# Kernel optimization log

Measured on AMD Instinct MI355X. Metric: run time of the kernel, lower is better.

## Reference

```python
import jax, jax.numpy as jnp
import numpy as np

E = 1024
H = 16
DH = E // H
FF = 4 * E
EPS = 1e-5


def _layer_norm(x, g, b):
    mu = jnp.mean(x, axis=-1, keepdims=True)
    var = jnp.var(x, axis=-1, keepdims=True)
    return (x - mu) * jax.lax.rsqrt(var + EPS) * g + b


def setup_inputs() -> dict:
    key = jax.random.key(0)
    ks = jax.random.split(key, 12)
    B, S = 2, 2048
    s_e = 1.0 / np.sqrt(E)
    s_f = 1.0 / np.sqrt(FF)
    return {
        "hidden_states": jax.random.normal(ks[0], (B, S, E), jnp.float32),
        "attention_mask": jnp.zeros((B, S), jnp.float32),
        "position_bias": jax.random.normal(ks[1], (H, S, S), jnp.float32) * 0.1,
        "Wq": jax.random.normal(ks[2], (E, E), jnp.float32) * s_e,
        "bq": jnp.zeros((E,), jnp.float32),
        "Wk": jax.random.normal(ks[3], (E, E), jnp.float32) * s_e,
        "bk": jnp.zeros((E,), jnp.float32),
        "Wv": jax.random.normal(ks[4], (E, E), jnp.float32) * s_e,
        "bv": jnp.zeros((E,), jnp.float32),
        "Wo": jax.random.normal(ks[5], (E, E), jnp.float32) * s_e,
        "bo": jnp.zeros((E,), jnp.float32),
        "ln1_g": jnp.ones((E,), jnp.float32),
        "ln1_b": jnp.zeros((E,), jnp.float32),
        "W1": jax.random.normal(ks[6], (E, FF), jnp.float32) * s_e,
        "b1": jnp.zeros((FF,), jnp.float32),
        "W2": jax.random.normal(ks[7], (FF, E), jnp.float32) * s_f,
        "b2": jnp.zeros((E,), jnp.float32),
        "ln2_g": jnp.ones((E,), jnp.float32),
        "ln2_b": jnp.zeros((E,), jnp.float32),
    }


def reference(hidden_states, attention_mask, position_bias, Wq, bq, Wk, bk, Wv, bv,
              Wo, bo, ln1_g, ln1_b, W1, b1, W2, b2, ln2_g, ln2_b):
    B, S, _ = hidden_states.shape
    x = hidden_states
    # QKV projections, split heads: [B, S, H, DH]
    q = (x @ Wq + bq).reshape(B, S, H, DH)
    k = (x @ Wk + bk).reshape(B, S, H, DH)
    v = (x @ Wv + bv).reshape(B, S, H, DH)
    # scores: [B, H, S, S]
    scores = jnp.einsum("bshd,bthd->bhst", q, k) / np.sqrt(DH).astype(np.float32)
    scores = scores + position_bias[None] + attention_mask[:, None, None, :]
    probs = jax.nn.softmax(scores, axis=-1)  # dropout is identity in eval
    ctx = jnp.einsum("bhst,bthd->bshd", probs, v).reshape(B, S, E)
    attn_out = ctx @ Wo + bo
    h = _layer_norm(x + attn_out, ln1_g, ln1_b)
    ffn = jax.nn.gelu(h @ W1 + b1, approximate=False) @ W2 + b2
    return _layer_norm(h + ffn, ln2_g, ln2_b)
```

## Files before the change

kernel.cpp:

```cpp
#include <hip/hip_runtime.h>
#include <stdint.h>

#define EDIM   1024
#define NHEAD  16
#define DHEAD  64
#define FFDIM  4096
#define SEQLEN 2048
#define NBATCH 2
#define MROWS  (NBATCH * SEQLEN)

typedef __attribute__((ext_vector_type(8))) short bf16x8;
typedef __attribute__((ext_vector_type(4))) float f32x4;

static __device__ __forceinline__ unsigned short f2bf(float f) {
    union { float f; uint32_t u; } v; v.f = f;
    return (unsigned short)((v.u + 0x7fffu + ((v.u >> 16) & 1u)) >> 16);
}

static __device__ __forceinline__ void gload16(const void* g, void* s) {
    __builtin_amdgcn_global_load_lds(
        (const __attribute__((address_space(1))) unsigned int*)g,
        (__attribute__((address_space(3))) unsigned int*)s,
        16, 0, 0);
}

__global__ void k_cast_bf16(const float* __restrict__ in, unsigned short* __restrict__ out, int n4) {
    int i = blockIdx.x * blockDim.x + threadIdx.x;
    if (i < n4) {
        float4 v = ((const float4*)in)[i];
        ushort4 o;
        o.x = f2bf(v.x); o.y = f2bf(v.y); o.z = f2bf(v.z); o.w = f2bf(v.w);
        ((ushort4*)out)[i] = o;
    }
}

__global__ void k_transpose_cast(const float* __restrict__ in, unsigned short* __restrict__ out,
                                 int R, int C) {
    __shared__ float tile[32][33];
    int c0 = blockIdx.x * 32, r0 = blockIdx.y * 32;
    int tx = threadIdx.x, ty = threadIdx.y;
    #pragma unroll
    for (int i = 0; i < 32; i += 8)
        tile[ty + i][tx] = in[(size_t)(r0 + ty + i) * C + c0 + tx];
    __syncthreads();
    #pragma unroll
    for (int i = 0; i < 32; i += 8)
        out[(size_t)(c0 + ty + i) * R + r0 + tx] = f2bf(tile[tx][ty + i]);
}

__global__ void k_transpose_v(const unsigned short* __restrict__ V, int vstride,
                              unsigned short* __restrict__ Vt) {
    __shared__ unsigned short tile[32][33];
    const int bh = blockIdx.z, b = bh >> 4, h = bh & 15;
    const int s0 = blockIdx.x * 32, d0 = blockIdx.y * 32;
    const int tx = threadIdx.x, ty = threadIdx.y;
    #pragma unroll
    for (int i = 0; i < 32; i += 8)
        tile[ty + i][tx] = V[(size_t)(b * SEQLEN + s0 + ty + i) * vstride + h * DHEAD + d0 + tx];
    __syncthreads();
    #pragma unroll
    for (int i = 0; i < 32; i += 8)
        Vt[((size_t)(b * NHEAD + h) * DHEAD + d0 + ty + i) * SEQLEN + s0 + tx] = tile[tx][ty + i];
}

__global__ void k_concat_bias(const float* __restrict__ bq, const float* __restrict__ bk,
                              const float* __restrict__ bv, float* __restrict__ out) {
    int i = blockIdx.x * 256 + threadIdx.x;
    const float* src = (i < 1024) ? bq : (i < 2048) ? bk : bv;
    out[i] = src[i & 1023];
}

template <int TBM, int TBN, int EPI>
__global__ __launch_bounds__(256, 2) void k_gemm(
    const unsigned short* __restrict__ A,
    const unsigned short* __restrict__ Bt,
    const float* __restrict__ bias,
    void* __restrict__ Cout, int M, int N, int K)
{
    constexpr int MR = TBM / 32, NR = TBN / 32;
    __shared__ __attribute__((aligned(16))) unsigned short Asm[TBM * 64];
    __shared__ __attribute__((aligned(16))) unsigned short Bsm[TBN * 64];

    const int row0 = blockIdx.y * TBM, col0 = blockIdx.x * TBN;
    const int t = threadIdx.x;
    const int lane = t & 63, w = t >> 6;
    const int wm = w >> 1, wn = w & 1;
    const int l15 = lane & 15, l4 = lane >> 4;
    const int sr = lane >> 3, sc = (lane & 7) * 8;

    f32x4 acc[MR][NR];
    #pragma unroll
    for (int m = 0; m < MR; ++m)
        #pragma unroll
        for (int n = 0; n < NR; ++n) acc[m][n] = (f32x4){0.f, 0.f, 0.f, 0.f};

    for (int k0 = 0; k0 < K; k0 += 64) {
        #pragma unroll
        for (int i = 0; i < TBM / 32; ++i) {
            const int r = w * (TBM / 4) + i * 8;
            gload16(A + (size_t)(row0 + r + sr) * K + k0 + sc, &Asm[r * 64]);
        }
        #pragma unroll
        for (int i = 0; i < TBN / 32; ++i) {
            const int r = w * (TBN / 4) + i * 8;
            gload16(Bt + (size_t)(col0 + r + sr) * K + k0 + sc, &Bsm[r * 64]);
        }
        __syncthreads();
        #pragma unroll
        for (int kk = 0; kk < 64; kk += 32) {
            bf16x8 af[MR], bf[NR];
            #pragma unroll
            for (int m = 0; m < MR; ++m)
                af[m] = *(const bf16x8*)&Asm[(wm * (TBM / 2) + m * 16 + l15) * 64 + kk + l4 * 8];
            #pragma unroll
            for (int n = 0; n < NR; ++n)
                bf[n] = *(const bf16x8*)&Bsm[(wn * (TBN / 2) + n * 16 + l15) * 64 + kk + l4 * 8];
            #pragma unroll
            for (int m = 0; m < MR; ++m)
                #pragma unroll
                for (int n = 0; n < NR; ++n)
                    acc[m][n] = __builtin_amdgcn_mfma_f32_16x16x32_bf16(af[m], bf[n], acc[m][n], 0, 0, 0);
        }
        __syncthreads();
    }

    #pragma unroll
    for (int m = 0; m < MR; ++m) {
        int rb = row0 + wm * (TBM / 2) + m * 16 + l4 * 4;
        #pragma unroll
        for (int n = 0; n < NR; ++n) {
            int c = col0 + wn * (TBN / 2) + n * 16 + l15;
            float bv = bias[c];
            #pragma unroll
            for (int i = 0; i < 4; ++i) {
                float v = acc[m][n][i] + bv;
                if (EPI == 1) v = 0.5f * v * (1.0f + erff(v * 0.70710678118654752f));
                if (EPI == 2) ((float*)Cout)[(size_t)(rb + i) * N + c] = v;
                else          ((unsigned short*)Cout)[(size_t)(rb + i) * N + c] = f2bf(v);
            }
        }
    }
}

__global__ __launch_bounds__(512, 2) void k_attn(
    const unsigned short* __restrict__ QKV,
    const unsigned short* __restrict__ Vt,
    const float* __restrict__ pbias,
    const float* __restrict__ mask,
    unsigned short* __restrict__ Ctx)
{
    __shared__ __attribute__((aligned(16))) unsigned short Ksm[2][64 * 72];
    __shared__ __attribute__((aligned(16))) unsigned short Vsm[2][64 * 72];
    __shared__ __attribute__((aligned(16))) unsigned short Psm[128 * 72];

    const int h = blockIdx.x;
    const int q0 = blockIdx.y * 64;
    const int t = threadIdx.x;
    const int lane = t & 63, w = t >> 6;
    const int wb = w & 1;
    const int wq = (w >> 1) * 16;
    const int l15 = lane & 15, l4 = lane >> 4;

    bf16x8 qf0, qf1;
    {
        const unsigned short* qp = QKV + (size_t)(wb * SEQLEN + q0 + wq + l15) * (3 * EDIM) + h * DHEAD + l4 * 8;
        qf0 = *(const bf16x8*)qp;
        qf1 = *(const bf16x8*)(qp + 32);
    }

    f32x4 oacc[4];
    #pragma unroll
    for (int nd = 0; nd < 4; ++nd) oacc[nd] = (f32x4){0.f, 0.f, 0.f, 0.f};
    float m_run[4] = {-1e30f, -1e30f, -1e30f, -1e30f};
    float l_run[4] = {0.f, 0.f, 0.f, 0.f};
    const int srow0 = q0 + wq + l4 * 4;
    const float* pbrow = pbias + ((size_t)h * SEQLEN + srow0) * SEQLEN;

    for (int kt = 0; kt < SEQLEN / 64; ++kt) {
        #pragma unroll
        for (int j = 0; j < 4; ++j) {
            int cid = j * 512 + t;
            int tile = cid >> 9;
            int r = (cid >> 3) & 63;
            int c = (cid & 7) * 8;
            int bb = tile & 1;
            if (tile < 2)
                *(float4*)&Ksm[bb][r * 72 + c] =
                    *(const float4*)(QKV + (size_t)(bb * SEQLEN + kt * 64 + r) * (3 * EDIM) + EDIM + h * DHEAD + c);
            else
                *(float4*)&Vsm[bb][r * 72 + c] =
                    *(const float4*)(Vt + ((size_t)((bb * NHEAD + h) * DHEAD + r)) * SEQLEN + kt * 64 + c);
        }
        __syncthreads();

        float pbv[4][4], mkv[4];
        #pragma unroll
        for (int n = 0; n < 4; ++n) {
            const int scol = kt * 64 + n * 16 + l15;
            mkv[n] = mask[wb * SEQLEN + scol];
            #pragma unroll
            for (int i = 0; i < 4; ++i)
                pbv[n][i] = pbrow[(size_t)i * SEQLEN + scol];
        }

        float p[4][4];
        float tmax[4] = {-1e30f, -1e30f, -1e30f, -1e30f};
        #pragma unroll
        for (int n = 0; n < 4; ++n) {
            bf16x8 kb0 = *(const bf16x8*)&Ksm[wb][(n * 16 + l15) * 72 + l4 * 8];
            bf16x8 kb1 = *(const bf16x8*)&Ksm[wb][(n * 16 + l15) * 72 + 32 + l4 * 8];
            f32x4 z = (f32x4){0.f, 0.f, 0.f, 0.f};
            z = __builtin_amdgcn_mfma_f32_16x16x32_bf16(qf0, kb0, z, 0, 0, 0);
            z = __builtin_amdgcn_mfma_f32_16x16x32_bf16(qf1, kb1, z, 0, 0, 0);
            #pragma unroll
            for (int i = 0; i < 4; ++i) {
                float v = z[i] * 0.125f + pbv[n][i] + mkv[n];
                p[n][i] = v;
                tmax[i] = fmaxf(tmax[i], v);
            }
        }
        #pragma unroll
        for (int i = 0; i < 4; ++i) {
            float mv = tmax[i];
            #pragma unroll
            for (int off = 1; off < 16; off <<= 1) mv = fmaxf(mv, __shfl_xor(mv, off, 64));
            float mnew = fmaxf(m_run[i], mv);
            float alpha = __expf(m_run[i] - mnew);
            m_run[i] = mnew;
            float sum = 0.f;
            #pragma unroll
            for (int n = 0; n < 4; ++n) { p[n][i] = __expf(p[n][i] - mnew); sum += p[n][i]; }
            #pragma unroll
            for (int off = 1; off < 16; off <<= 1) sum += __shfl_xor(sum, off, 64);
            l_run[i] = l_run[i] * alpha + sum;
            #pragma unroll
            for (int nd = 0; nd < 4; ++nd) oacc[nd][i] *= alpha;
        }
        #pragma unroll
        for (int n = 0; n < 4; ++n)
            #pragma unroll
            for (int i = 0; i < 4; ++i)
                Psm[(w * 16 + l4 * 4 + i) * 72 + n * 16 + l15] = f2bf(p[n][i]);
        #pragma unroll
        for (int kk = 0; kk < 2; ++kk) {
            bf16x8 pa = *(const bf16x8*)&Psm[(w * 16 + l15) * 72 + kk * 32 + l4 * 8];
            #pragma unroll
            for (int nd = 0; nd < 4; ++nd) {
                bf16x8 vf = *(const bf16x8*)&Vsm[wb][(nd * 16 + l15) * 72 + kk * 32 + l4 * 8];
                oacc[nd] = __builtin_amdgcn_mfma_f32_16x16x32_bf16(pa, vf, oacc[nd], 0, 0, 0);
            }
        }
        __syncthreads();
    }

    #pragma unroll
    for (int nd = 0; nd < 4; ++nd)
        #pragma unroll
        for (int i = 0; i < 4; ++i) {
            float v = oacc[nd][i] / l_run[i];
            Ctx[(size_t)(wb * SEQLEN + q0 + wq + l4 * 4 + i) * EDIM + h * DHEAD + nd * 16 + l15] = f2bf(v);
        }
}

template <int WRITE_BF>
__global__ __launch_bounds__(256) void k_ln(
    const float* __restrict__ X, const float* __restrict__ T,
    const float* __restrict__ gam, const float* __restrict__ bet,
    float* __restrict__ Of, unsigned short* __restrict__ Ob)
{
    const int r = blockIdx.x;
    const int t = threadIdx.x;
    const size_t base = (size_t)r * EDIM + t * 4;
    float4 xv = *(const float4*)(X + base);
    float4 tv = *(const float4*)(T + base);
    float4 s = make_float4(xv.x + tv.x, xv.y + tv.y, xv.z + tv.z, xv.w + tv.w);
    float sum = s.x + s.y + s.z + s.w;
    float sq  = s.x * s.x + s.y * s.y + s.z * s.z + s.w * s.w;
    #pragma unroll
    for (int off = 1; off < 64; off <<= 1) {
        sum += __shfl_xor(sum, off, 64);
        sq  += __shfl_xor(sq,  off, 64);
    }
    __shared__ float red[8];
    const int lane = t & 63, w = t >> 6;
    if (lane == 0) { red[w] = sum; red[4 + w] = sq; }
    __syncthreads();
    sum = red[0] + red[1] + red[2] + red[3];
    sq  = red[4] + red[5] + red[6] + red[7];
    const float mu = sum * (1.0f / EDIM);
    const float var = sq * (1.0f / EDIM) - mu * mu;
    const float rs = rsqrtf(var + 1e-5f);
    float4 gv = *(const float4*)(gam + t * 4);
    float4 bv = *(const float4*)(bet + t * 4);
    float4 o = make_float4((s.x - mu) * rs * gv.x + bv.x,
                           (s.y - mu) * rs * gv.y + bv.y,
                           (s.z - mu) * rs * gv.z + bv.z,
                           (s.w - mu) * rs * gv.w + bv.w);
    *(float4*)(Of + base) = o;
    if (WRITE_BF) {
        ushort4 ob;
        ob.x = f2bf(o.x); ob.y = f2bf(o.y); ob.z = f2bf(o.z); ob.w = f2bf(o.w);
        *(ushort4*)(Ob + base) = ob;
    }
}

extern "C" void kernel_launch(void* const* d_in, const int* in_sizes, int n_in,
                              void* d_out, int out_size, void* d_ws, size_t ws_size,
                              hipStream_t stream) {
    const float* x    = (const float*)d_in[0];
    const float* mask = (const float*)d_in[1];
    const float* pb   = (const float*)d_in[2];
    const float* Wq = (const float*)d_in[3];  const float* bq = (const float*)d_in[4];
    const float* Wk = (const float*)d_in[5];  const float* bk = (const float*)d_in[6];
    const float* Wv = (const float*)d_in[7];  const float* bv = (const float*)d_in[8];
    const float* Wo = (const float*)d_in[9];  const float* bo = (const float*)d_in[10];
    const float* g1 = (const float*)d_in[11]; const float* be1 = (const float*)d_in[12];
    const float* W1 = (const float*)d_in[13]; const float* b1 = (const float*)d_in[14];
    const float* W2 = (const float*)d_in[15]; const float* b2 = (const float*)d_in[16];
    const float* g2 = (const float*)d_in[17]; const float* be2 = (const float*)d_in[18];
    float* out = (float*)d_out;

    char* ws = (char*)d_ws;
    const size_t MB = 1024 * 1024;
    unsigned short* qkv  = (unsigned short*)(ws + 0);
    unsigned short* gbf  = (unsigned short*)(ws + 0);
    unsigned short* xb   = (unsigned short*)(ws + 24 * MB);
    unsigned short* vt   = (unsigned short*)(ws + 24 * MB);
    unsigned short* wqt  = (unsigned short*)(ws + 32 * MB);
    unsigned short* wkt  = (unsigned short*)(ws + 34 * MB);
    unsigned short* wvt  = (unsigned short*)(ws + 36 * MB);
    unsigned short* wot  = (unsigned short*)(ws + 38 * MB);
    unsigned short* w1t  = (unsigned short*)(ws + 40 * MB);
    unsigned short* w2t  = (unsigned short*)(ws + 48 * MB);
    float*          bcat = (float*)(ws + 56 * MB);
    unsigned short* ctxb = (unsigned short*)(ws + 56 * MB);
    float*          t1   = (float*)(ws + 64 * MB);
    float*          hf   = (float*)(ws + 80 * MB);
    unsigned short* hb   = (unsigned short*)(ws + 96 * MB);

    const dim3 b256(256);
    const dim3 tb(32, 8);

    k_cast_bf16<<<dim3(MROWS * EDIM / 4 / 256), b256, 0, stream>>>(x, xb, MROWS * EDIM / 4);
    k_transpose_cast<<<dim3(EDIM / 32, EDIM / 32), tb, 0, stream>>>(Wq, wqt, EDIM, EDIM);
    k_transpose_cast<<<dim3(EDIM / 32, EDIM / 32), tb, 0, stream>>>(Wk, wkt, EDIM, EDIM);
    k_transpose_cast<<<dim3(EDIM / 32, EDIM / 32), tb, 0, stream>>>(Wv, wvt, EDIM, EDIM);
    k_transpose_cast<<<dim3(EDIM / 32, EDIM / 32), tb, 0, stream>>>(Wo, wot, EDIM, EDIM);
    k_transpose_cast<<<dim3(FFDIM / 32, EDIM / 32), tb, 0, stream>>>(W1, w1t, EDIM, FFDIM);
    k_transpose_cast<<<dim3(EDIM / 32, FFDIM / 32), tb, 0, stream>>>(W2, w2t, FFDIM, EDIM);
    k_concat_bias<<<dim3(12), b256, 0, stream>>>(bq, bk, bv, bcat);

    k_gemm<128, 128, 0><<<dim3(3 * EDIM / 128, MROWS / 128), b256, 0, stream>>>(
        xb, wqt, bcat, qkv, MROWS, 3 * EDIM, EDIM);
    k_transpose_v<<<dim3(SEQLEN / 32, DHEAD / 32, NBATCH * NHEAD), tb, 0, stream>>>(
        qkv + 2 * EDIM, 3 * EDIM, vt);

    k_attn<<<dim3(NHEAD, SEQLEN / 64), dim3(512), 0, stream>>>(qkv, vt, pb, mask, ctxb);

    k_gemm<128, 64, 2><<<dim3(EDIM / 64, MROWS / 128), b256, 0, stream>>>(
        ctxb, wot, bo, t1, MROWS, EDIM, EDIM);
    k_ln<1><<<dim3(MROWS), b256, 0, stream>>>(x, t1, g1, be1, hf, hb);
    k_gemm<128, 128, 1><<<dim3(FFDIM / 128, MROWS / 128), b256, 0, stream>>>(
        hb, w1t, b1, gbf, MROWS, FFDIM, EDIM);
    k_gemm<128, 64, 2><<<dim3(EDIM / 64, MROWS / 128), b256, 0, stream>>>(
        gbf, w2t, b2, t1, MROWS, EDIM, FFDIM);
    k_ln<0><<<dim3(MROWS), b256, 0, stream>>>(hf, t1, g2, be2, out, nullptr);
    (void)in_sizes; (void)n_in; (void)out_size; (void)ws_size;
}
```

Baseline: 420.7 us.

## Restructure attention kernel: per-batch blocks, 128-wide KV tiles, swizzled async LDS loads

Each attention block now handles a single batch element via a third grid dimension, with 256 threads instead of 512. It processes 128 keys per iteration, which halves the number of loop iterations and barriers. K and V tiles are loaded with global_load_lds direct-to-LDS copies using an XOR column swizzle, replacing register-staged stores and padded rows. The position bias and mask are pre-added and fused into an FMA with the scores. The risk is that position_bias, which is shared across batches, is now read by two separate blocks that are far apart in the launch order, which may double its dominant HBM traffic.

```diff
diff --git a/kernel.cpp b/kernel.cpp
--- a/kernel.cpp
+++ b/kernel.cpp
@@ -142,28 +142,33 @@
     }
 }
 
-__global__ __launch_bounds__(512, 2) void k_attn(
+#define KVB 128
+#define PLD 136
+
+__global__ __launch_bounds__(256, 3) void k_attn(
     const unsigned short* __restrict__ QKV,
     const unsigned short* __restrict__ Vt,
     const float* __restrict__ pbias,
     const float* __restrict__ mask,
     unsigned short* __restrict__ Ctx)
 {
-    __shared__ __attribute__((aligned(16))) unsigned short Ksm[2][64 * 72];
-    __shared__ __attribute__((aligned(16))) unsigned short Vsm[2][64 * 72];
-    __shared__ __attribute__((aligned(16))) unsigned short Psm[128 * 72];
+    __shared__ __attribute__((aligned(16))) unsigned short Ksm[KVB * 64];
+    __shared__ __attribute__((aligned(16))) unsigned short Vsm[64 * KVB];
+    __shared__ __attribute__((aligned(16))) unsigned short Psm[64 * PLD];
 
     const int h = blockIdx.x;
     const int q0 = blockIdx.y * 64;
+    const int b = blockIdx.z;
     const int t = threadIdx.x;
     const int lane = t & 63, w = t >> 6;
-    const int wb = w & 1;
-    const int wq = (w >> 1) * 16;
     const int l15 = lane & 15, l4 = lane >> 4;
+
+    const int kr_off = lane >> 3, kc = lane & 7;
+    const int vr_off = lane >> 4, vc = lane & 15;
 
     bf16x8 qf0, qf1;
     {
-        const unsigned short* qp = QKV + (size_t)(wb * SEQLEN + q0 + wq + l15) * (3 * EDIM) + h * DHEAD + l4 * 8;
+        const unsigned short* qp = QKV + (size_t)(b * SEQLEN + q0 + w * 16 + l15) * (3 * EDIM) + h * DHEAD + l4 * 8;
         qf0 = *(const bf16x8*)qp;
         qf1 = *(const bf16x8*)(qp + 32);
     }
@@ -173,48 +178,54 @@
     for (int nd = 0; nd < 4; ++nd) oacc[nd] = (f32x4){0.f, 0.f, 0.f, 0.f};
     float m_run[4] = {-1e30f, -1e30f, -1e30f, -1e30f};
     float l_run[4] = {0.f, 0.f, 0.f, 0.f};
-    const int srow0 = q0 + wq + l4 * 4;
+    const int srow0 = q0 + w * 16 + l4 * 4;
     const float* pbrow = pbias + ((size_t)h * SEQLEN + srow0) * SEQLEN;
-
-    for (int kt = 0; kt < SEQLEN / 64; ++kt) {
+    const float* mrow  = mask + b * SEQLEN;
+
+    for (int kt = 0; kt < SEQLEN / KVB; ++kt) {
         #pragma unroll
         for (int j = 0; j < 4; ++j) {
-            int cid = j * 512 + t;
-            int tile = cid >> 9;
-            int r = (cid >> 3) & 63;
-            int c = (cid & 7) * 8;
-            int bb = tile & 1;
-            if (tile < 2)
-                *(float4*)&Ksm[bb][r * 72 + c] =
-                    *(const float4*)(QKV + (size_t)(bb * SEQLEN + kt * 64 + r) * (3 * EDIM) + EDIM + h * DHEAD + c);
-            else
-                *(float4*)&Vsm[bb][r * 72 + c] =
-                    *(const float4*)(Vt + ((size_t)((bb * NHEAD + h) * DHEAD + r)) * SEQLEN + kt * 64 + c);
+            const int issue = w * 4 + j;
+            {
+                const int r = issue * 8 + kr_off;
+                const int c = (kc ^ (r & 7)) * 8;
+                gload16(QKV + (size_t)(b * SEQLEN + kt * KVB + r) * (3 * EDIM) + EDIM + h * DHEAD + c,
+                        &Ksm[issue * 512]);
+            }
+            {
+                const int r = issue * 4 + vr_off;
+                const int c = (vc ^ (r & 7)) * 8;
+                gload16(Vt + ((size_t)((b * NHEAD + h) * DHEAD + r)) * SEQLEN + kt * KVB + c,
+                        &Vsm[issue * 512]);
+            }
         }
         __syncthreads();
 
-        float pbv[4][4], mkv[4];
-        #pragma unroll
-        for (int n = 0; n < 4; ++n) {
-            const int scol = kt * 64 + n * 16 + l15;
-            mkv[n] = mask[wb * SEQLEN + scol];
+        float pq[8][4];
+        #pragma unroll
+        for (int n = 0; n < 8; ++n) {
+            const int scol = kt * KVB + n * 16 + l15;
+            const float mk = mrow[scol];
             #pragma unroll
             for (int i = 0; i < 4; ++i)
-                pbv[n][i] = pbrow[(size_t)i * SEQLEN + scol];
-        }
-
-        float p[4][4];
+                pq[n][i] = pbrow[(size_t)i * SEQLEN + scol] + mk;
+        }
+
+        float p[8][4];
         float tmax[4] = {-1e30f, -1e30f, -1e30f, -1e30f};
         #pragma unroll
-        for (int n = 0; n < 4; ++n) {
-            bf16x8 kb0 = *(const bf16x8*)&Ksm[wb][(n * 16 + l15) * 72 + l4 * 8];
-            bf16x8 kb1 = *(const bf16x8*)&Ksm[wb][(n * 16 + l15) * 72 + 32 + l4 * 8];
+        for (int n = 0; n < 8; ++n) {
+            const int rk = n * 16 + l15;
+            const int ch0 = (l4 ^ (l15 & 7)) * 8;
+            const int ch1 = ((4 + l4) ^ (l15 & 7)) * 8;
+            bf16x8 kb0 = *(const bf16x8*)&Ksm[rk * 64 + ch0];
+            bf16x8 kb1 = *(const bf16x8*)&Ksm[rk * 64 + ch1];
             f32x4 z = (f32x4){0.f, 0.f, 0.f, 0.f};
             z = __builtin_amdgcn_mfma_f32_16x16x32_bf16(qf0, kb0, z, 0, 0, 0);
             z = __builtin_amdgcn_mfma_f32_16x16x32_bf16(qf1, kb1, z, 0, 0, 0);
             #pragma unroll
             for (int i = 0; i < 4; ++i) {
-                float v = z[i] * 0.125f + pbv[n][i] + mkv[n];
+                float v = fmaf(z[i], 0.125f, pq[n][i]);
                 p[n][i] = v;
                 tmax[i] = fmaxf(tmax[i], v);
             }
@@ -229,7 +240,7 @@
             m_run[i] = mnew;
             float sum = 0.f;
             #pragma unroll
-            for (int n = 0; n < 4; ++n) { p[n][i] = __expf(p[n][i] - mnew); sum += p[n][i]; }
+            for (int n = 0; n < 8; ++n) { p[n][i] = __expf(p[n][i] - mnew); sum += p[n][i]; }
             #pragma unroll
             for (int off = 1; off < 16; off <<= 1) sum += __shfl_xor(sum, off, 64);
             l_run[i] = l_run[i] * alpha + sum;
@@ -237,16 +248,18 @@
             for (int nd = 0; nd < 4; ++nd) oacc[nd][i] *= alpha;
         }
         #pragma unroll
-        for (int n = 0; n < 4; ++n)
+        for (int n = 0; n < 8; ++n)
             #pragma unroll
             for (int i = 0; i < 4; ++i)
-                Psm[(w * 16 + l4 * 4 + i) * 72 + n * 16 + l15] = f2bf(p[n][i]);
-        #pragma unroll
-        for (int kk = 0; kk < 2; ++kk) {
-            bf16x8 pa = *(const bf16x8*)&Psm[(w * 16 + l15) * 72 + kk * 32 + l4 * 8];
+                Psm[(w * 16 + l4 * 4 + i) * PLD + n * 16 + l15] = f2bf(p[n][i]);
+        #pragma unroll
+        for (int ks = 0; ks < 4; ++ks) {
+            bf16x8 pa = *(const bf16x8*)&Psm[(w * 16 + l15) * PLD + ks * 32 + l4 * 8];
             #pragma unroll
             for (int nd = 0; nd < 4; ++nd) {
-                bf16x8 vf = *(const bf16x8*)&Vsm[wb][(nd * 16 + l15) * 72 + kk * 32 + l4 * 8];
+                const int rd = nd * 16 + l15;
+                const int ch = ((ks * 4 + l4) ^ (l15 & 7)) * 8;
+                bf16x8 vf = *(const bf16x8*)&Vsm[rd * KVB + ch];
                 oacc[nd] = __builtin_amdgcn_mfma_f32_16x16x32_bf16(pa, vf, oacc[nd], 0, 0, 0);
             }
         }
@@ -258,7 +271,7 @@
         #pragma unroll
         for (int i = 0; i < 4; ++i) {
             float v = oacc[nd][i] / l_run[i];
-            Ctx[(size_t)(wb * SEQLEN + q0 + wq + l4 * 4 + i) * EDIM + h * DHEAD + nd * 16 + l15] = f2bf(v);
+            Ctx[(size_t)(b * SEQLEN + q0 + w * 16 + l4 * 4 + i) * EDIM + h * DHEAD + nd * 16 + l15] = f2bf(v);
         }
 }
 
@@ -355,7 +368,7 @@
     k_transpose_v<<<dim3(SEQLEN / 32, DHEAD / 32, NBATCH * NHEAD), tb, 0, stream>>>(
         qkv + 2 * EDIM, 3 * EDIM, vt);
 
-    k_attn<<<dim3(NHEAD, SEQLEN / 64), dim3(512), 0, stream>>>(qkv, vt, pb, mask, ctxb);
+    k_attn<<<dim3(NHEAD, SEQLEN / 64, NBATCH), b256, 0, stream>>>(qkv, vt, pb, mask, ctxb);
 
     k_gemm<128, 64, 2><<<dim3(EDIM / 64, MROWS / 128), b256, 0, stream>>>(
         ctxb, wot, bo, t1, MROWS, EDIM, EDIM);
```

Result: slower. 698.7 us (+66.1%).

## Drop LDS staging in attention, read K/V directly from global per wave

Applied to the files above, without the earlier changes.

The attention kernel no longer stages K and V tiles in shared memory with block-wide barriers. Each wave now loads its MFMA K and V fragments straight from global memory (relying on L1/L2 reuse across waves) and keeps only a per-wave P buffer. Blocks shrink to 256 threads covering one batch and 64 queries, and the grid is reordered so blocks sharing a head run together. Position bias and mask are folded into the MFMA accumulator init, and the 1/sqrt(d) scale is pre-applied to Q before it is rounded to bf16, which adds a small rounding difference. Dropping the barriers removes sync stalls but raises global and cache traffic for K and V.

```diff
diff --git a/kernel.cpp b/kernel.cpp
--- a/kernel.cpp
+++ b/kernel.cpp
@@ -142,30 +142,39 @@
     }
 }
 
-__global__ __launch_bounds__(512, 2) void k_attn(
+__global__ __launch_bounds__(256, 4) void k_attn(
     const unsigned short* __restrict__ QKV,
     const unsigned short* __restrict__ Vt,
     const float* __restrict__ pbias,
     const float* __restrict__ mask,
     unsigned short* __restrict__ Ctx)
 {
-    __shared__ __attribute__((aligned(16))) unsigned short Ksm[2][64 * 72];
-    __shared__ __attribute__((aligned(16))) unsigned short Vsm[2][64 * 72];
-    __shared__ __attribute__((aligned(16))) unsigned short Psm[128 * 72];
-
-    const int h = blockIdx.x;
-    const int q0 = blockIdx.y * 64;
+    __shared__ __attribute__((aligned(16))) unsigned short Psm[4][16 * 72];
+
+    const int b = blockIdx.x & 1, qt = blockIdx.x >> 1;
+    const int h = blockIdx.y;
     const int t = threadIdx.x;
     const int lane = t & 63, w = t >> 6;
-    const int wb = w & 1;
-    const int wq = (w >> 1) * 16;
     const int l15 = lane & 15, l4 = lane >> 4;
+    const int qrow = qt * 64 + w * 16;
+
+    const unsigned short* Kg = QKV + (size_t)(b * SEQLEN) * (3 * EDIM) + EDIM + h * DHEAD;
+    const unsigned short* Vg = Vt + (size_t)((b * NHEAD + h) * DHEAD) * SEQLEN;
 
     bf16x8 qf0, qf1;
     {
-        const unsigned short* qp = QKV + (size_t)(wb * SEQLEN + q0 + wq + l15) * (3 * EDIM) + h * DHEAD + l4 * 8;
-        qf0 = *(const bf16x8*)qp;
-        qf1 = *(const bf16x8*)(qp + 32);
+        const unsigned short* qp = QKV + (size_t)(b * SEQLEN + qrow + l15) * (3 * EDIM) + h * DHEAD + l4 * 8;
+        bf16x8 r0 = *(const bf16x8*)qp;
+        bf16x8 r1 = *(const bf16x8*)(qp + 32);
+        #pragma unroll
+        for (int e = 0; e < 8; ++e) {
+            union { uint32_t u; float f; } c0, c1;
+            c0.u = (uint32_t)(unsigned short)r0[e] << 16;
+            c1.u = (uint32_t)(unsigned short)r1[e] << 16;
+            r0[e] = (short)f2bf(c0.f * 0.125f);
+            r1[e] = (short)f2bf(c1.f * 0.125f);
+        }
+        qf0 = r0; qf1 = r1;
     }
 
     f32x4 oacc[4];
@@ -173,50 +182,29 @@
     for (int nd = 0; nd < 4; ++nd) oacc[nd] = (f32x4){0.f, 0.f, 0.f, 0.f};
     float m_run[4] = {-1e30f, -1e30f, -1e30f, -1e30f};
     float l_run[4] = {0.f, 0.f, 0.f, 0.f};
-    const int srow0 = q0 + wq + l4 * 4;
-    const float* pbrow = pbias + ((size_t)h * SEQLEN + srow0) * SEQLEN;
+    const float* pbrow = pbias + ((size_t)h * SEQLEN + qrow + l4 * 4) * SEQLEN;
+    const float* mrow  = mask + b * SEQLEN;
 
     for (int kt = 0; kt < SEQLEN / 64; ++kt) {
-        #pragma unroll
-        for (int j = 0; j < 4; ++j) {
-            int cid = j * 512 + t;
-            int tile = cid >> 9;
-            int r = (cid >> 3) & 63;
-            int c = (cid & 7) * 8;
-            int bb = tile & 1;
-            if (tile < 2)
-                *(float4*)&Ksm[bb][r * 72 + c] =
-                    *(const float4*)(QKV + (size_t)(bb * SEQLEN + kt * 64 + r) * (3 * EDIM) + EDIM + h * DHEAD + c);
-            else
-                *(float4*)&Vsm[bb][r * 72 + c] =
-                    *(const float4*)(Vt + ((size_t)((bb * NHEAD + h) * DHEAD + r)) * SEQLEN + kt * 64 + c);
-        }
-        __syncthreads();
-
-        float pbv[4][4], mkv[4];
-        #pragma unroll
-        for (int n = 0; n < 4; ++n) {
-            const int scol = kt * 64 + n * 16 + l15;
-            mkv[n] = mask[wb * SEQLEN + scol];
-            #pragma unroll
-            for (int i = 0; i < 4; ++i)
-                pbv[n][i] = pbrow[(size_t)i * SEQLEN + scol];
-        }
-
+        const int kbase = kt * 64;
         float p[4][4];
         float tmax[4] = {-1e30f, -1e30f, -1e30f, -1e30f};
         #pragma unroll
         for (int n = 0; n < 4; ++n) {
-            bf16x8 kb0 = *(const bf16x8*)&Ksm[wb][(n * 16 + l15) * 72 + l4 * 8];
-            bf16x8 kb1 = *(const bf16x8*)&Ksm[wb][(n * 16 + l15) * 72 + 32 + l4 * 8];
-            f32x4 z = (f32x4){0.f, 0.f, 0.f, 0.f};
+            const int scol = kbase + n * 16 + l15;
+            f32x4 z;
+            const float mk = mrow[scol];
+            #pragma unroll
+            for (int i = 0; i < 4; ++i) z[i] = pbrow[(size_t)i * SEQLEN + scol] + mk;
+            const unsigned short* kp = Kg + (size_t)scol * (3 * EDIM) + l4 * 8;
+            bf16x8 kb0 = *(const bf16x8*)kp;
+            bf16x8 kb1 = *(const bf16x8*)(kp + 32);
             z = __builtin_amdgcn_mfma_f32_16x16x32_bf16(qf0, kb0, z, 0, 0, 0);
             z = __builtin_amdgcn_mfma_f32_16x16x32_bf16(qf1, kb1, z, 0, 0, 0);
             #pragma unroll
             for (int i = 0; i < 4; ++i) {
-                float v = z[i] * 0.125f + pbv[n][i] + mkv[n];
-                p[n][i] = v;
-                tmax[i] = fmaxf(tmax[i], v);
+                p[n][i] = z[i];
+                tmax[i] = fmaxf(tmax[i], z[i]);
             }
         }
         #pragma unroll
@@ -240,17 +228,16 @@
         for (int n = 0; n < 4; ++n)
             #pragma unroll
             for (int i = 0; i < 4; ++i)
-                Psm[(w * 16 + l4 * 4 + i) * 72 + n * 16 + l15] = f2bf(p[n][i]);
+                Psm[w][(l4 * 4 + i) * 72 + n * 16 + l15] = f2bf(p[n][i]);
         #pragma unroll
         for (int kk = 0; kk < 2; ++kk) {
-            bf16x8 pa = *(const bf16x8*)&Psm[(w * 16 + l15) * 72 + kk * 32 + l4 * 8];
+            bf16x8 pa = *(const bf16x8*)&Psm[w][l15 * 72 + kk * 32 + l4 * 8];
             #pragma unroll
             for (int nd = 0; nd < 4; ++nd) {
-                bf16x8 vf = *(const bf16x8*)&Vsm[wb][(nd * 16 + l15) * 72 + kk * 32 + l4 * 8];
+                bf16x8 vf = *(const bf16x8*)(Vg + (size_t)(nd * 16 + l15) * SEQLEN + kbase + kk * 32 + l4 * 8);
                 oacc[nd] = __builtin_amdgcn_mfma_f32_16x16x32_bf16(pa, vf, oacc[nd], 0, 0, 0);
             }
         }
-        __syncthreads();
     }
 
     #pragma unroll
@@ -258,7 +245,7 @@
         #pragma unroll
         for (int i = 0; i < 4; ++i) {
             float v = oacc[nd][i] / l_run[i];
-            Ctx[(size_t)(wb * SEQLEN + q0 + wq + l4 * 4 + i) * EDIM + h * DHEAD + nd * 16 + l15] = f2bf(v);
+            Ctx[(size_t)(b * SEQLEN + qrow + l4 * 4 + i) * EDIM + h * DHEAD + nd * 16 + l15] = f2bf(v);
         }
 }
 
@@ -355,7 +342,7 @@
     k_transpose_v<<<dim3(SEQLEN / 32, DHEAD / 32, NBATCH * NHEAD), tb, 0, stream>>>(
         qkv + 2 * EDIM, 3 * EDIM, vt);
 
-    k_attn<<<dim3(NHEAD, SEQLEN / 64), dim3(512), 0, stream>>>(qkv, vt, pb, mask, ctxb);
+    k_attn<<<dim3(2 * SEQLEN / 64, NHEAD), b256, 0, stream>>>(qkv, vt, pb, mask, ctxb);
 
     k_gemm<128, 64, 2><<<dim3(EDIM / 64, MROWS / 128), b256, 0, stream>>>(
         ctxb, wot, bo, t1, MROWS, EDIM, EDIM);
```

After: 559.4 us. +33.0%, slower.
